# Optimization experiments

Measured on AMD Instinct MI355X. Metric: run time of the kernel, lower is better.

The kernel has to match this reference:

```python
import jax, jax.numpy as jnp
import numpy as np

B, I, O, K = 4096, 1024, 1024, 16

def setup_inputs() -> dict:
    key = jax.random.key(0)
    k1, k2 = jax.random.split(key)
    x = jax.random.normal(k1, (B, I), dtype=jnp.float32)
    weights = jax.random.normal(k2, (O, I, K), dtype=jnp.float32)
    bias = jnp.zeros((O,), dtype=jnp.float32)
    centers = jnp.linspace(-1.0, 1.0, K, dtype=jnp.float32)
    widths = jnp.full((K,), 0.1, dtype=jnp.float32)
    return {"x": x, "weights": weights, "bias": bias, "centers": centers, "widths": widths}

def reference(x, weights, bias, centers, widths):
    # Gaussian RBF basis: [B, I, K]
    diff = x[:, :, None] - centers[None, None, :]
    kernels = jnp.exp(-(diff ** 2) / (2.0 * widths[None, None, :] ** 2))
    # Contraction over input_dim and num_kernels (GEMM-equivalent)
    out = jnp.einsum('bik,oik->bo', kernels, weights)
    return out + bias
```

## Files before the change

### kernel.cpp

```cpp
#include <hip/hip_runtime.h>
#include <hip/hip_bf16.h>


#define B_DIM 4096
#define I_DIM 1024
#define O_DIM 1024
#define NK 16
#define KD (I_DIM * NK)

#define BM 128
#define BN 64
#define BK 64

typedef __attribute__((ext_vector_type(8))) __bf16 bf16x8;
typedef __attribute__((ext_vector_type(4))) float f32x4;
typedef __attribute__((ext_vector_type(8))) unsigned short u16x8;

typedef const __attribute__((address_space(1))) unsigned short gu16;
typedef __attribute__((address_space(3))) unsigned short lu16;

static __device__ __forceinline__ unsigned short f2bf(float f) {
  unsigned u = __float_as_uint(f);
  u += 0x7FFFu + ((u >> 16) & 1u);
  return (unsigned short)(u >> 16);
}

__global__ void __launch_bounds__(256) rbf_feat(const float* __restrict__ x,
                                                unsigned short* __restrict__ feat,
                                                const float* __restrict__ centers,
                                                const float* __restrict__ widths) {
  const int idx = blockIdx.x * 256 + threadIdx.x;
  const float xv = x[idx];
  u16x8 lo, hi;
#pragma unroll
  for (int k = 0; k < 16; ++k) {
    const float c = centers[k];
    const float w = widths[k];
    const float s = -0.5f * __builtin_amdgcn_rcpf(w * w);
    const float d = xv - c;
    const unsigned short h = f2bf(__expf(d * d * s));
    if (k < 8) lo[k] = h; else hi[k - 8] = h;
  }
  u16x8* dst = (u16x8*)(feat + (size_t)idx * 16);
  dst[0] = lo;
  dst[1] = hi;
}

__global__ void __launch_bounds__(256) cvt_w(const float4* __restrict__ w,
                                             u16x8* __restrict__ wb) {
  const size_t i = (size_t)blockIdx.x * 256 + threadIdx.x;
  const float4 a = w[2 * i];
  const float4 b = w[2 * i + 1];
  u16x8 o;
  o[0] = f2bf(a.x); o[1] = f2bf(a.y); o[2] = f2bf(a.z); o[3] = f2bf(a.w);
  o[4] = f2bf(b.x); o[5] = f2bf(b.y); o[6] = f2bf(b.z); o[7] = f2bf(b.w);
  wb[i] = o;
}

__global__ void __launch_bounds__(256, 2) gemm_bt(const unsigned short* __restrict__ A,
                                                  const unsigned short* __restrict__ Bm,
                                                  const float* __restrict__ bias,
                                                  float* __restrict__ C) {
  __shared__ unsigned short sA[BM * BK];
  __shared__ unsigned short sB[BN * BK];

  const int t = threadIdx.x;
  const int bm = blockIdx.x;
  const int bn = blockIdx.y;
  const int wid = t >> 6, l = t & 63;
  const int wr = wid >> 1, wc = wid & 1;
  const int lm = l & 15, lk = l >> 4;

  const unsigned short* aG = A + (size_t)bm * BM * KD;
  const unsigned short* bG = Bm + (size_t)bn * BN * KD;

  const int st_rowA = t >> 3, st_slot = t & 7;
  (void)st_rowA; (void)st_slot;

  f32x4 acc[4][2];
#pragma unroll
  for (int mi = 0; mi < 4; ++mi)
#pragma unroll
    for (int ni = 0; ni < 2; ++ni)
      acc[mi][ni] = (f32x4){0.f, 0.f, 0.f, 0.f};

  for (int kt = 0; kt < KD; kt += BK) {
#pragma unroll
    for (int j = 0; j < 4; ++j) {
      const int chunk = j * 256 + t;
      const int row = chunk >> 3, slot = chunk & 7;
      const int c = slot ^ (row & 7);
      __builtin_amdgcn_global_load_lds(
          (gu16*)(aG + (size_t)row * KD + kt + c * 8),
          (lu16*)(sA + chunk * 8), 16, 0, 0);
    }
#pragma unroll
    for (int j = 0; j < 2; ++j) {
      const int chunk = j * 256 + t;
      const int row = chunk >> 3, slot = chunk & 7;
      const int c = slot ^ (row & 7);
      __builtin_amdgcn_global_load_lds(
          (gu16*)(bG + (size_t)row * KD + kt + c * 8),
          (lu16*)(sB + chunk * 8), 16, 0, 0);
    }
    __syncthreads();

#pragma unroll
    for (int kk = 0; kk < 2; ++kk) {
      const int s = (kk * 4 + lk) ^ (lm & 7);
      bf16x8 af[4], bfr[2];
#pragma unroll
      for (int mi = 0; mi < 4; ++mi)
        af[mi] = *(const bf16x8*)(sA + (wr * 64 + mi * 16 + lm) * BK + s * 8);
#pragma unroll
      for (int ni = 0; ni < 2; ++ni)
        bfr[ni] = *(const bf16x8*)(sB + (wc * 32 + ni * 16 + lm) * BK + s * 8);
#pragma unroll
      for (int mi = 0; mi < 4; ++mi)
#pragma unroll
        for (int ni = 0; ni < 2; ++ni)
          acc[mi][ni] = __builtin_amdgcn_mfma_f32_16x16x32_bf16(af[mi], bfr[ni],
                                                                acc[mi][ni], 0, 0, 0);
    }
    __syncthreads();
  }

#pragma unroll
  for (int ni = 0; ni < 2; ++ni) {
    const int col = bn * BN + wc * 32 + ni * 16 + lm;
    const float bv = bias[col];
#pragma unroll
    for (int mi = 0; mi < 4; ++mi) {
      const int row0 = bm * BM + wr * 64 + mi * 16 + lk * 4;
#pragma unroll
      for (int j = 0; j < 4; ++j)
        C[(size_t)(row0 + j) * O_DIM + col] = acc[mi][ni][j] + bv;
    }
  }
}

extern "C" void kernel_launch(void* const* d_in, const int* in_sizes, int n_in,
                              void* d_out, int out_size, void* d_ws, size_t ws_size,
                              hipStream_t stream) {
  const float* x = (const float*)d_in[0];
  const float* w = (const float*)d_in[1];
  const float* bias = (const float*)d_in[2];
  const float* centers = (const float*)d_in[3];
  const float* widths = (const float*)d_in[4];
  float* out = (float*)d_out;

  unsigned short* feat = (unsigned short*)d_ws;
  unsigned short* wb = (unsigned short*)((char*)d_ws + (size_t)B_DIM * KD * 2);

  rbf_feat<<<(B_DIM * I_DIM) / 256, 256, 0, stream>>>(x, feat, centers, widths);
  cvt_w<<<(O_DIM * KD) / (256 * 8), 256, 0, stream>>>((const float4*)w, (u16x8*)wb);

  dim3 grid(B_DIM / BM, O_DIM / BN);
  gemm_bt<<<grid, 256, 0, stream>>>(feat, wb, bias, out);
}
```

Measured before the change: 227.5 us.

## Add 256x256 split-K pipelined GEMM with partial-sum reduction

Adds a new GEMM kernel with 512 threads, 256x256 output tiles, double-buffered LDS staging split into half-tiles, and prefetching interleaved with MFMA phases using barriers and setprio. K is split four ways across blockIdx.z so the grid fills the device. A separate reduce kernel sums the four partials and adds bias. This raises data reuse per tile and overlaps loads with compute, at the cost of extra partial-buffer traffic and a reduction pass. The old GEMM remains as a fallback when the workspace is too small.

Measured after the change: 214.3 us. -5.8%, faster.

```diff
diff --git a/kernel.cpp b/kernel.cpp
--- a/kernel.cpp
+++ b/kernel.cpp
@@ -8,10 +8,7 @@
 #define NK 16
 #define KD (I_DIM * NK)
 
-#define BM 128
-#define BN 64
-#define BK 64
-
+typedef unsigned short u16;
 typedef __attribute__((ext_vector_type(8))) __bf16 bf16x8;
 typedef __attribute__((ext_vector_type(4))) float f32x4;
 typedef __attribute__((ext_vector_type(8))) unsigned short u16x8;
@@ -19,14 +16,14 @@
 typedef const __attribute__((address_space(1))) unsigned short gu16;
 typedef __attribute__((address_space(3))) unsigned short lu16;
 
-static __device__ __forceinline__ unsigned short f2bf(float f) {
+static __device__ __forceinline__ u16 f2bf(float f) {
   unsigned u = __float_as_uint(f);
   u += 0x7FFFu + ((u >> 16) & 1u);
-  return (unsigned short)(u >> 16);
+  return (u16)(u >> 16);
 }
 
 __global__ void __launch_bounds__(256) rbf_feat(const float* __restrict__ x,
-                                                unsigned short* __restrict__ feat,
+                                                u16* __restrict__ feat,
                                                 const float* __restrict__ centers,
                                                 const float* __restrict__ widths) {
   const int idx = blockIdx.x * 256 + threadIdx.x;
@@ -38,7 +35,7 @@
     const float w = widths[k];
     const float s = -0.5f * __builtin_amdgcn_rcpf(w * w);
     const float d = xv - c;
-    const unsigned short h = f2bf(__expf(d * d * s));
+    const u16 h = f2bf(__expf(d * d * s));
     if (k < 8) lo[k] = h; else hi[k - 8] = h;
   }
   u16x8* dst = (u16x8*)(feat + (size_t)idx * 16);
@@ -57,25 +54,152 @@
   wb[i] = o;
 }
 
-__global__ void __launch_bounds__(256, 2) gemm_bt(const unsigned short* __restrict__ A,
-                                                  const unsigned short* __restrict__ Bm,
-                                                  const float* __restrict__ bias,
-                                                  float* __restrict__ C) {
-  __shared__ unsigned short sA[BM * BK];
-  __shared__ unsigned short sB[BN * BK];
+static __device__ __forceinline__ void stage_half(const u16* __restrict__ g,
+                                                  u16* __restrict__ lds, int t) {
+#pragma unroll
+  for (int j = 0; j < 2; ++j) {
+    const int chunk = j * 512 + t;
+    const int row = chunk >> 3, slot = chunk & 7;
+    const int c = slot ^ (row & 7);
+    __builtin_amdgcn_global_load_lds((gu16*)(g + (size_t)row * KD + c * 8),
+                                     (lu16*)(lds + chunk * 8), 16, 0, 0);
+  }
+}
+
+#define NT 64
+
+__global__ void __launch_bounds__(512, 2)
+gemm8(const u16* __restrict__ A, const u16* __restrict__ Bm,
+      float* __restrict__ part) {
+  __shared__ u16 sA[2][2][128 * 64];
+  __shared__ u16 sB[2][2][128 * 64];
 
   const int t = threadIdx.x;
   const int bm = blockIdx.x;
   const int bn = blockIdx.y;
+  const int kz = blockIdx.z;
+  const int wid = t >> 6, l = t & 63;
+  const int wr = wid >> 2, wc = wid & 3;
+  const int lm = l & 15, lk = l >> 4;
+
+  const u16* aT = A + (size_t)(bm * 256) * KD + kz * 4096;
+  const u16* bT = Bm + (size_t)(bn * 256) * KD + kz * 4096;
+
+  f32x4 acc[8][4];
+#pragma unroll
+  for (int i = 0; i < 8; ++i)
+#pragma unroll
+    for (int j = 0; j < 4; ++j)
+      acc[i][j] = (f32x4){0.f, 0.f, 0.f, 0.f};
+
+  stage_half(aT, &sA[0][0][0], t);
+  stage_half(aT + (size_t)128 * KD, &sA[0][1][0], t);
+  stage_half(bT, &sB[0][0][0], t);
+  stage_half(bT + (size_t)128 * KD, &sB[0][1][0], t);
+  stage_half(bT + 64, &sB[1][0][0], t);
+  stage_half(aT + 64, &sA[1][0][0], t);
+  asm volatile("s_waitcnt vmcnt(4)" ::: "memory");
+  __builtin_amdgcn_s_barrier();
+
+  for (int T = 0; T < NT; ++T) {
+    const int c = T & 1;
+#pragma unroll
+    for (int p = 0; p < 4; ++p) {
+      const int qa = p & 1, qb = p >> 1;
+      bf16x8 af[4][2], bfr[2][2];
+#pragma unroll
+      for (int mi = 0; mi < 4; ++mi)
+#pragma unroll
+        for (int kk = 0; kk < 2; ++kk)
+          af[mi][kk] = *(const bf16x8*)&sA[c][qa][
+              (wr * 64 + mi * 16 + lm) * 64 + (((kk * 4 + lk) ^ (lm & 7)) * 8)];
+#pragma unroll
+      for (int ni = 0; ni < 2; ++ni)
+#pragma unroll
+        for (int kk = 0; kk < 2; ++kk)
+          bfr[ni][kk] = *(const bf16x8*)&sB[c][qb][
+              (wc * 32 + ni * 16 + lm) * 64 + (((kk * 4 + lk) ^ (lm & 7)) * 8)];
+      if (p == 0 && T + 1 < NT)
+        stage_half(aT + (size_t)128 * KD + (T + 1) * 64, &sA[(T + 1) & 1][1][0], t);
+      if (p == 1 && T + 1 < NT)
+        stage_half(bT + (size_t)128 * KD + (T + 1) * 64, &sB[(T + 1) & 1][1][0], t);
+      if (p == 2 && T + 2 < NT)
+        stage_half(bT + (T + 2) * 64, &sB[T & 1][0][0], t);
+      if (p == 3 && T + 2 < NT)
+        stage_half(aT + (T + 2) * 64, &sA[T & 1][0][0], t);
+
+      __builtin_amdgcn_s_barrier();
+      asm volatile("s_waitcnt lgkmcnt(0)" ::: "memory");
+      __builtin_amdgcn_sched_barrier(0);
+      __builtin_amdgcn_s_setprio(1);
+#pragma unroll
+      for (int mi = 0; mi < 4; ++mi)
+#pragma unroll
+        for (int ni = 0; ni < 2; ++ni)
+#pragma unroll
+          for (int kk = 0; kk < 2; ++kk)
+            acc[qa * 4 + mi][qb * 2 + ni] = __builtin_amdgcn_mfma_f32_16x16x32_bf16(
+                af[mi][kk], bfr[ni][kk], acc[qa * 4 + mi][qb * 2 + ni], 0, 0, 0);
+      __builtin_amdgcn_s_setprio(0);
+      if (p == 3) {
+        if (T + 2 < NT) asm volatile("s_waitcnt vmcnt(4)" ::: "memory");
+        else            asm volatile("s_waitcnt vmcnt(0)" ::: "memory");
+      }
+      __builtin_amdgcn_s_barrier();
+    }
+  }
+
+  float* pW = part + (size_t)kz * ((size_t)B_DIM * O_DIM);
+#pragma unroll
+  for (int qa = 0; qa < 2; ++qa)
+#pragma unroll
+    for (int mi = 0; mi < 4; ++mi)
+#pragma unroll
+      for (int qb = 0; qb < 2; ++qb)
+#pragma unroll
+        for (int ni = 0; ni < 2; ++ni) {
+          const int row0 = bm * 256 + qa * 128 + wr * 64 + mi * 16 + lk * 4;
+          const int col = bn * 256 + qb * 128 + wc * 32 + ni * 16 + lm;
+#pragma unroll
+          for (int j = 0; j < 4; ++j)
+            pW[(size_t)(row0 + j) * O_DIM + col] = acc[qa * 4 + mi][qb * 2 + ni][j];
+        }
+}
+
+__global__ void __launch_bounds__(256) reduce4(const float4* __restrict__ p,
+                                               const float4* __restrict__ bias4,
+                                               float4* __restrict__ out) {
+  const int i = blockIdx.x * 256 + threadIdx.x;
+  const size_t s = (size_t)B_DIM * O_DIM / 4;
+  const float4 a = p[i], b = p[i + s], c = p[i + 2 * s], d = p[i + 3 * s];
+  const float4 bb = bias4[i & 255];
+  float4 r;
+  r.x = a.x + b.x + c.x + d.x + bb.x;
+  r.y = a.y + b.y + c.y + d.y + bb.y;
+  r.z = a.z + b.z + c.z + d.z + bb.z;
+  r.w = a.w + b.w + c.w + d.w + bb.w;
+  out[i] = r;
+}
+
+#define BM 128
+#define BN 64
+#define BK 64
+
+__global__ void __launch_bounds__(256, 2) gemm_bt(const u16* __restrict__ A,
+                                                  const u16* __restrict__ Bm,
+                                                  const float* __restrict__ bias,
+                                                  float* __restrict__ C) {
+  __shared__ u16 sA[BM * BK];
+  __shared__ u16 sB[BN * BK];
+
+  const int t = threadIdx.x;
+  const int bm = blockIdx.x, bn = blockIdx.y;
   const int wid = t >> 6, l = t & 63;
   const int wr = wid >> 1, wc = wid & 1;
   const int lm = l & 15, lk = l >> 4;
 
-  const unsigned short* aG = A + (size_t)bm * BM * KD;
-  const unsigned short* bG = Bm + (size_t)bn * BN * KD;
-
-  const int st_rowA = t >> 3, st_slot = t & 7;
-  (void)st_rowA; (void)st_slot;
+  const u16* aG = A + (size_t)bm * BM * KD;
+  const u16* bG = Bm + (size_t)bn * BN * KD;
 
   f32x4 acc[4][2];
 #pragma unroll
@@ -90,21 +214,18 @@
       const int chunk = j * 256 + t;
       const int row = chunk >> 3, slot = chunk & 7;
       const int c = slot ^ (row & 7);
-      __builtin_amdgcn_global_load_lds(
-          (gu16*)(aG + (size_t)row * KD + kt + c * 8),
-          (lu16*)(sA + chunk * 8), 16, 0, 0);
+      __builtin_amdgcn_global_load_lds((gu16*)(aG + (size_t)row * KD + kt + c * 8),
+                                       (lu16*)(sA + chunk * 8), 16, 0, 0);
     }
 #pragma unroll
     for (int j = 0; j < 2; ++j) {
       const int chunk = j * 256 + t;
       const int row = chunk >> 3, slot = chunk & 7;
       const int c = slot ^ (row & 7);
-      __builtin_amdgcn_global_load_lds(
-          (gu16*)(bG + (size_t)row * KD + kt + c * 8),
-          (lu16*)(sB + chunk * 8), 16, 0, 0);
+      __builtin_amdgcn_global_load_lds((gu16*)(bG + (size_t)row * KD + kt + c * 8),
+                                       (lu16*)(sB + chunk * 8), 16, 0, 0);
     }
     __syncthreads();
-
 #pragma unroll
     for (int kk = 0; kk < 2; ++kk) {
       const int s = (kk * 4 + lk) ^ (lm & 7);
@@ -149,12 +270,22 @@
   const float* widths = (const float*)d_in[4];
   float* out = (float*)d_out;
 
-  unsigned short* feat = (unsigned short*)d_ws;
-  unsigned short* wb = (unsigned short*)((char*)d_ws + (size_t)B_DIM * KD * 2);
+  u16* feat = (u16*)d_ws;
+  u16* wb = (u16*)((char*)d_ws + (size_t)B_DIM * KD * 2);
+  float* part = (float*)((char*)d_ws + (size_t)B_DIM * KD * 2 + (size_t)O_DIM * KD * 2);
 
   rbf_feat<<<(B_DIM * I_DIM) / 256, 256, 0, stream>>>(x, feat, centers, widths);
   cvt_w<<<(O_DIM * KD) / (256 * 8), 256, 0, stream>>>((const float4*)w, (u16x8*)wb);
 
-  dim3 grid(B_DIM / BM, O_DIM / BN);
-  gemm_bt<<<grid, 256, 0, stream>>>(feat, wb, bias, out);
-}
+  const size_t need = (size_t)B_DIM * KD * 2 + (size_t)O_DIM * KD * 2 +
+                      4ull * B_DIM * O_DIM * 4;
+  if (ws_size >= need) {
+    dim3 grid(B_DIM / 256, O_DIM / 256, 4);
+    gemm8<<<grid, 512, 0, stream>>>(feat, wb, part);
+    reduce4<<<(B_DIM * O_DIM / 4) / 256, 256, 0, stream>>>(
+        (const float4*)part, (const float4*)bias, (float4*)out);
+  } else {
+    dim3 grid(B_DIM / BM, O_DIM / BN);
+    gemm_bt<<<grid, 256, 0, stream>>>(feat, wb, bias, out);
+  }
+}
```
